# Kernel tuning notes

Measured on AMD Instinct MI355X. Metric: run time of the kernel, lower is better.

Reference implementation:

```python
import jax, jax.numpy as jnp
import numpy as np

BETA = 0.25  # commitment cost
EPS = 1e-10


def _vq_layer(xf, cb):
    # xf: [M, D] flattened features, cb: [K, D] codebook
    K = cb.shape[0]
    M = xf.shape[0]
    d = (jnp.sum(xf * xf, axis=-1, keepdims=True)
         - 2.0 * (xf @ cb.T)
         + jnp.sum(cb * cb, axis=-1))
    idx = jnp.argmin(d, axis=-1)          # [M]
    q = cb[idx]                           # [M, D]
    # commitment + codebook loss (VQ-VAE)
    commit = jnp.mean((jax.lax.stop_gradient(q) - xf) ** 2)
    cbloss = jnp.mean((q - jax.lax.stop_gradient(xf)) ** 2)
    loss = cbloss + BETA * commit
    # straight-through estimator
    q_st = xf + jax.lax.stop_gradient(q - xf)
    # codebook usage perplexity
    counts = jnp.zeros((K,), dtype=xf.dtype).at[idx].add(1.0)
    p = counts / M
    perplexity = jnp.exp(-jnp.sum(p * jnp.log(p + EPS)))
    return q_st, idx, loss, perplexity


def setup_inputs() -> dict:
    key = jax.random.key(0)
    k1, k2 = jax.random.split(key)
    B, N, D, H, W, K = 32, 4, 128, 32, 32, 1024
    x = jax.random.normal(k1, (B, N * D, H, W), dtype=jnp.float32)
    codebooks = jax.random.normal(k2, (N, K, D), dtype=jnp.float32)
    return {"x": x, "codebooks": codebooks}


def reference(x, codebooks):
    B, C, H, W = x.shape
    N, K, D = codebooks.shape
    assert C == N * D
    M = B * H * W
    # [B, N*D, H, W] -> [N, M, D]
    xs = x.reshape(B, N, D, H, W).transpose(1, 0, 3, 4, 2).reshape(N, M, D)
    q, idx, loss, perp = jax.vmap(_vq_layer)(xs, codebooks)
    # quantized_cat: [N, M, D] -> [B, N*D, H, W]  (cat along channel dim)
    quantized_cat = (q.reshape(N, B, H, W, D)
                      .transpose(1, 0, 4, 2, 3)
                      .reshape(B, N * D, H, W))
    # indices_cat: [N, M] -> [B, N, H, W]
    indices_cat = idx.reshape(N, B, H, W).transpose(1, 0, 2, 3)
    return quantized_cat, indices_cat, loss, perp
```

## Files before the change

kernel.cpp:

```cpp
#include <hip/hip_runtime.h>

#define B_ 32
#define N_ 4
#define D_ 128
#define M_ 32768
#define K_ 1024

#define IDX_OFF 16777216
#define LOSS_OFF 16908288
#define PERP_OFF 16908292

#define WS_LOSS 0
#define WS_CNT 1024
#define WS_ENORM 8192
#define WS_BPACK_F 16384
#define BPACK_LAYER_US 262144
#define WS_IDX 540672

#define SBIAS 384.0f
#define MARGIN 0.012f

typedef __bf16 bf16x8 __attribute__((ext_vector_type(8)));
typedef float f32x4 __attribute__((ext_vector_type(4)));

union FragU {
  bf16x8 v;
  ushort u16[8];
  uint4 q;
};

__device__ __forceinline__ ushort bf16_hi_rne(float f, float* hif) {
  uint u = __float_as_uint(f);
  uint r = (u + 0x7fffu + ((u >> 16) & 1u)) >> 16;
  *hif = __uint_as_float(r << 16);
  return (ushort)r;
}
__device__ __forceinline__ ushort bf16_rne(float f) {
  uint u = __float_as_uint(f);
  return (ushort)((u + 0x7fffu + ((u >> 16) & 1u)) >> 16);
}

__device__ __forceinline__ void gload_lds16(const void* g, void* l) {
  __builtin_amdgcn_global_load_lds(
      (const __attribute__((address_space(1))) unsigned int*)g,
      (__attribute__((address_space(3))) unsigned int*)l, 16, 0, 0);
}

__global__ __launch_bounds__(256) void vq_pack(const float* __restrict__ cb,
                                               float* __restrict__ ws) {
  __shared__ ushort Hs[16 * 132];
  __shared__ ushort Ls[16 * 132];
  __shared__ float Ps[256];
  int blk = blockIdx.x, tid = threadIdx.x;
  if (blk < 256) {
    int n = blk >> 6, tile = blk & 63;
    int c = tid >> 4, f = tid & 15;
    const float* src = cb + ((size_t)(n * K_ + tile * 16 + c)) * D_ + f * 8;
    float4 v0 = *(const float4*)src;
    float4 v1 = *(const float4*)(src + 4);
    float v[8] = {v0.x, v0.y, v0.z, v0.w, v1.x, v1.y, v1.z, v1.w};
    float ss = 0.f;
#pragma unroll
    for (int j = 0; j < 8; ++j) {
      float hif;
      Hs[c * 132 + f * 8 + j] = bf16_hi_rne(v[j], &hif);
      Ls[c * 132 + f * 8 + j] = bf16_rne(v[j] - hif);
      ss = fmaf(v[j], v[j], ss);
    }
    Ps[c * 16 + f] = ss;
    __syncthreads();
    if (tid < 16) {
      float s = 0.f;
#pragma unroll
      for (int j = 0; j < 16; ++j) s += Ps[tid * 16 + j];
      ws[WS_ENORM + n * K_ + tile * 16 + tid] = SBIAS - 0.5f * s;
    }
    int s = tid >> 6, lane = tid & 63;
    int code = lane & 15, dstart = s * 32 + ((lane >> 4) << 3);
    FragU fh, fl;
#pragma unroll
    for (int j = 0; j < 8; ++j) {
      fh.u16[j] = Hs[code * 132 + dstart + j];
      fl.u16[j] = Ls[code * 132 + dstart + j];
    }
    ushort* dst = (ushort*)(ws + WS_BPACK_F) + (size_t)n * BPACK_LAYER_US +
                  ((size_t)(tile * 4 + s) * 2) * 512 + lane * 8;
    *(uint4*)dst = fh.q;
    *(uint4*)(dst + 512) = fl.q;
  } else {
#pragma unroll
    for (int i = 0; i < 20; ++i) ws[i * 256 + tid] = 0.f;
  }
}

__global__ __launch_bounds__(256, 4) void vq_score(const float* __restrict__ x,
                                                   const float* __restrict__ cb,
                                                   float* __restrict__ ws,
                                                   float* __restrict__ out) {
  __shared__ alignas(16) ushort Bsm[18432];
  const int tid = threadIdx.x;
  const int bid = blockIdx.x;
  const int n = bid >> 8;
  const int mblk = bid & 255;
  const int b = mblk >> 3;
  const int hw0 = (mblk & 7) << 7;

  const int lane = tid & 63, w = tid >> 6;
  const int quad = lane >> 4, l15 = lane & 15;

  const float* xbase = x + (size_t)((b * 4 + n) * 128) * 1024 + hw0;
  const float* cbn = cb + (size_t)n * K_ * D_;
  const float* enB = ws + WS_ENORM + n * K_;
  const uint4* gsrc = (const uint4*)((ushort*)(ws + WS_BPACK_F) + (size_t)n * BPACK_LAYER_US);
  uint4* Bsm4 = (uint4*)Bsm;

  char* ext = (char*)Bsm + 32768;
  int* sIdx = (int*)ext;
  float* dist = (float*)(ext + 512);
  int* list = (int*)(ext + 1024);
  int* lcnt = (int*)(ext + 1536);
  double* xrowd = (double*)(ext + 1544);
  double* rd = (double*)(ext + 2568);
  int* rk = (int*)(ext + 2600);

  if (tid == 0) *lcnt = 0;

  bf16x8 ahi[2][4], alo[2][4];
#pragma unroll
  for (int set = 0; set < 2; ++set) {
    const int hwl = w * 32 + set * 16 + l15;
    float xs = 0.f;
#pragma unroll
    for (int s = 0; s < 4; ++s) {
      const int dbase = s * 32 + quad * 8;
      FragU fh, fl;
#pragma unroll
      for (int j = 0; j < 8; ++j) {
        float v = xbase[(size_t)(dbase + j) * 1024 + hwl];
        xs = fmaf(v, v, xs);
        float hif;
        fh.u16[j] = bf16_hi_rne(v, &hif);
        fl.u16[j] = bf16_rne(v - hif);
      }
      ahi[set][s] = fh.v;
      alo[set][s] = fl.v;
    }
    xs += __shfl_xor(xs, 16, 64);
    xs += __shfl_xor(xs, 32, 64);
    if (lane < 16) dist[w * 32 + set * 16 + l15] = xs;
  }

  uint best[8], best2[8], keyp[8];
#pragma unroll
  for (int i = 0; i < 8; ++i) { best[i] = 0u; best2[i] = 0u; keyp[i] = 0u; }

#pragma unroll
  for (int i = 0; i < 4; ++i)
    gload_lds16(gsrc + i * 256 + w * 64 + lane, Bsm4 + i * 256 + w * 64);

#pragma unroll 1
  for (int c = 0; c < 32; ++c) {
    __syncthreads();
    if (c < 31) {
      const uint4* src = gsrc + (c + 1) * 1024;
      uint4* dst = Bsm4 + ((c + 1) & 1) * 1024;
#pragma unroll
      for (int i = 0; i < 4; ++i)
        gload_lds16(src + i * 256 + w * 64 + lane, dst + i * 256 + w * 64);
    }
    const ushort* Bcur = Bsm + (c & 1) * 8192;
#pragma unroll
    for (int tin = 0; tin < 2; ++tin) {
      const int t = c * 2 + tin;
      const uint tinv = (uint)(63 - t);
      float en = enB[t * 16 + l15];
      bf16x8 bh[4], bl[4];
#pragma unroll
      for (int s = 0; s < 4; ++s) {
        const ushort* p = Bcur + ((tin * 4 + s) * 2) * 512 + lane * 8;
        bh[s] = ((const FragU*)p)->v;
        bl[s] = ((const FragU*)(p + 512))->v;
      }
      f32x4 acc[2];
#pragma unroll
      for (int set = 0; set < 2; ++set) acc[set] = (f32x4){0.f, 0.f, 0.f, 0.f};
#pragma unroll
      for (int s = 0; s < 4; ++s) {
#pragma unroll
        for (int set = 0; set < 2; ++set)
          acc[set] = __builtin_amdgcn_mfma_f32_16x16x32_bf16(ahi[set][s], bh[s], acc[set], 0, 0, 0);
#pragma unroll
        for (int set = 0; set < 2; ++set)
          acc[set] = __builtin_amdgcn_mfma_f32_16x16x32_bf16(ahi[set][s], bl[s], acc[set], 0, 0, 0);
#pragma unroll
        for (int set = 0; set < 2; ++set)
          acc[set] = __builtin_amdgcn_mfma_f32_16x16x32_bf16(alo[set][s], bh[s], acc[set], 0, 0, 0);
      }
#pragma unroll
      for (int i = 0; i < 8; ++i) {
        uint k = keyp[i], ob = best[i];
        uint mn = k < ob ? k : ob;
        best[i] = k > ob ? k : ob;
        if (mn > best2[i]) best2[i] = mn;
      }
#pragma unroll
      for (int set = 0; set < 2; ++set) {
#pragma unroll
        for (int r = 0; r < 4; ++r) {
          float sb = acc[set][r] + en;
          keyp[set * 4 + r] = (__float_as_uint(sb) & 0xFFFFFFC0u) | tinv;
        }
      }
    }
  }
#pragma unroll
  for (int i = 0; i < 8; ++i) {
    uint k = keyp[i], ob = best[i];
    uint mn = k < ob ? k : ob;
    best[i] = k > ob ? k : ob;
    if (mn > best2[i]) best2[i] = mn;
  }
  __syncthreads();

  uint* sS = (uint*)Bsm;
  uint* sS2 = (uint*)((char*)Bsm + 8704);
#pragma unroll
  for (int set = 0; set < 2; ++set) {
#pragma unroll
    for (int r = 0; r < 4; ++r) {
      int m = w * 32 + set * 16 + quad * 4 + r;
      sS[m * 17 + l15] = best[set * 4 + r];
      sS2[m * 17 + l15] = best2[set * 4 + r];
    }
  }
  __syncthreads();

  if (tid < 128) {
    int m = tid;
    uint g1 = 0, g2 = 0;
    int gi = 0;
#pragma unroll 4
    for (int li = 0; li < 16; ++li) {
      uint key = sS[m * 17 + li];
      uint sb = key >> 6;
      int kk = (int)(63u - (key & 63u)) * 16 + li;
      if (sb > g1) { g2 = g1; g1 = sb; gi = kk; }
      else {
        if (sb == g1 && kk < gi) gi = kk;
        if (sb > g2) g2 = sb;
      }
      uint sb2 = sS2[m * 17 + li] >> 6;
      if (sb2 > g2) g2 = sb2;
    }
    sIdx[m] = gi;
    float s1f = __uint_as_float(g1 << 6);
    dist[m] = dist[m] - 2.0f * (s1f - SBIAS);
    float gap = s1f - __uint_as_float(g2 << 6);
    if (gap < MARGIN) {
      int pos = atomicAdd(lcnt, 1);
      list[pos] = m;
    }
  }
  __syncthreads();

  const int cnt = *lcnt;
  for (int i = 0; i < cnt; ++i) {
    const int m = list[i];
    if (tid < 128) xrowd[tid] = (double)xbase[(size_t)tid * 1024 + m];
    __syncthreads();
    double bd = 1e300;
    int bk = 0;
#pragma unroll 1
    for (int j = 0; j < 4; ++j) {
      const int k = tid * 4 + j;
      const float4* er = (const float4*)(cbn + (size_t)k * D_);
      double d = 0.0;
#pragma unroll 8
      for (int c4 = 0; c4 < 32; ++c4) {
        float4 e = er[c4];
        double d0 = xrowd[c4 * 4 + 0] - (double)e.x;
        double d1 = xrowd[c4 * 4 + 1] - (double)e.y;
        double d2 = xrowd[c4 * 4 + 2] - (double)e.z;
        double d3 = xrowd[c4 * 4 + 3] - (double)e.w;
        d = fma(d0, d0, d);
        d = fma(d1, d1, d);
        d = fma(d2, d2, d);
        d = fma(d3, d3, d);
      }
      if (d < bd) { bd = d; bk = k; }
    }
#pragma unroll
    for (int off = 32; off; off >>= 1) {
      double od = __shfl_down(bd, off, 64);
      int ok = __shfl_down(bk, off, 64);
      if (od < bd || (od == bd && ok < bk)) { bd = od; bk = ok; }
    }
    if (lane == 0) { rd[w] = bd; rk[w] = bk; }
    __syncthreads();
    if (tid == 0) {
      double gb = rd[0];
      int gk = rk[0];
      for (int t = 1; t < 4; ++t)
        if (rd[t] < gb || (rd[t] == gb && rk[t] < gk)) { gb = rd[t]; gk = rk[t]; }
      sIdx[m] = gk;
      dist[m] = (float)gb;
    }
    __syncthreads();
  }

  if (tid < 128) {
    int bi = sIdx[tid];
    int gpos = (b * 4 + n) * 1024 + hw0 + tid;
    out[IDX_OFF + gpos] = (float)bi;
    ((int*)(ws + WS_IDX))[gpos] = bi;
    atomicAdd(ws + WS_CNT + n * K_ + bi, 1.0f);
  }
  float lp = (tid < 128) ? dist[tid] : 0.f;
#pragma unroll
  for (int off = 32; off; off >>= 1) lp += __shfl_down(lp, off, 64);
  if (lane == 0 && w < 2) atomicAdd(ws + WS_LOSS + n, lp);
}

__global__ __launch_bounds__(256) void vq_write(const float* __restrict__ cb,
                                                const float* __restrict__ ws,
                                                float* __restrict__ out) {
  __shared__ float Qs[32 * 128];
  __shared__ int sIdx[128];
  const int tid = threadIdx.x;
  const int bid = blockIdx.x;
  const int n = bid >> 8;
  const int mblk = bid & 255;
  const int b = mblk >> 3;
  const int hw0 = (mblk & 7) << 7;
  const float* cbn = cb + (size_t)n * K_ * D_;
  const int* ig = (const int*)(ws + WS_IDX) + (b * 4 + n) * 1024 + hw0;
  if (tid < 128) sIdx[tid] = ig[tid];
  __syncthreads();
  float* out0 = out + (size_t)((b * 4 + n) * 128) * 1024 + hw0;
#pragma unroll 1
  for (int q = 0; q < 4; ++q) {
    const int m = tid & 127, part = tid >> 7;
    const float* src = cbn + (size_t)sIdx[m] * D_ + q * 32 + part * 16;
#pragma unroll
    for (int i = 0; i < 4; ++i) {
      float4 v = ((const float4*)src)[i];
      int dl = part * 16 + i * 4;
      Qs[(dl + 0) * 128 + m] = v.x;
      Qs[(dl + 1) * 128 + m] = v.y;
      Qs[(dl + 2) * 128 + m] = v.z;
      Qs[(dl + 3) * 128 + m] = v.w;
    }
    __syncthreads();
#pragma unroll
    for (int it = 0; it < 4; ++it) {
      int e = it * 256 + tid;
      int m4 = (e & 31) * 4;
      int dl = e >> 5;
      float4 v = *(float4*)(Qs + dl * 128 + m4);
      *(float4*)(out0 + (size_t)(q * 32 + dl) * 1024 + m4) = v;
    }
    __syncthreads();
  }
}

__global__ void vq_finalize(const float* __restrict__ ws, float* __restrict__ out) {
  int n = blockIdx.x;
  int t = threadIdx.x;
  const float* counts = ws + WS_CNT + n * K_;
  float s = 0.f;
  for (int k = t; k < K_; k += 256) {
    float p = counts[k] * (1.0f / 32768.0f);
    s += p * logf(p + 1e-10f);
  }
  __shared__ float red[4];
#pragma unroll
  for (int off = 32; off; off >>= 1) s += __shfl_down(s, off, 64);
  if ((t & 63) == 0) red[t >> 6] = s;
  __syncthreads();
  if (t == 0) {
    s = red[0] + red[1] + red[2] + red[3];
    out[PERP_OFF + n] = expf(-s);
    out[LOSS_OFF + n] = 1.25f * ws[WS_LOSS + n] / 4194304.0f;
  }
}

extern "C" void kernel_launch(void* const* d_in, const int* in_sizes, int n_in,
                              void* d_out, int out_size, void* d_ws, size_t ws_size,
                              hipStream_t stream) {
  const float* x = (const float*)d_in[0];
  const float* cb = (const float*)d_in[1];
  float* out = (float*)d_out;
  float* ws = (float*)d_ws;
  vq_pack<<<257, 256, 0, stream>>>(cb, ws);
  vq_score<<<1024, 256, 0, stream>>>(x, cb, ws, out);
  vq_write<<<1024, 256, 0, stream>>>(cb, ws, out);
  vq_finalize<<<4, 256, 0, stream>>>(ws, out);
}
```

Measured before the change: 296.9 us.

## Fuse scoring and quantized write into one kernel with 256-row blocks

```diff
diff --git a/kernel.cpp b/kernel.cpp
--- a/kernel.cpp
+++ b/kernel.cpp
@@ -15,7 +15,6 @@
 #define WS_ENORM 8192
 #define WS_BPACK_F 16384
 #define BPACK_LAYER_US 262144
-#define WS_IDX 540672
 
 #define SBIAS 384.0f
 #define MARGIN 0.012f
@@ -93,17 +92,17 @@
   }
 }
 
-__global__ __launch_bounds__(256, 4) void vq_score(const float* __restrict__ x,
-                                                   const float* __restrict__ cb,
-                                                   float* __restrict__ ws,
-                                                   float* __restrict__ out) {
-  __shared__ alignas(16) ushort Bsm[18432];
+__global__ __launch_bounds__(512, 4) void vq_main(const float* __restrict__ x,
+                                                  const float* __restrict__ cb,
+                                                  float* __restrict__ ws,
+                                                  float* __restrict__ out) {
+  __shared__ alignas(16) char Lds[37120];
   const int tid = threadIdx.x;
   const int bid = blockIdx.x;
-  const int n = bid >> 8;
-  const int mblk = bid & 255;
-  const int b = mblk >> 3;
-  const int hw0 = (mblk & 7) << 7;
+  const int n = bid >> 7;
+  const int mblk = bid & 127;
+  const int b = mblk >> 2;
+  const int hw0 = (mblk & 3) << 8;
 
   const int lane = tid & 63, w = tid >> 6;
   const int quad = lane >> 4, l15 = lane & 15;
@@ -112,16 +111,18 @@
   const float* cbn = cb + (size_t)n * K_ * D_;
   const float* enB = ws + WS_ENORM + n * K_;
   const uint4* gsrc = (const uint4*)((ushort*)(ws + WS_BPACK_F) + (size_t)n * BPACK_LAYER_US);
-  uint4* Bsm4 = (uint4*)Bsm;
-
-  char* ext = (char*)Bsm + 32768;
+
+  ushort* Bsm = (ushort*)Lds;
+  uint4* Bsm4 = (uint4*)Lds;
+  char* ext = Lds + 32896;
   int* sIdx = (int*)ext;
-  float* dist = (float*)(ext + 512);
-  int* list = (int*)(ext + 1024);
-  int* lcnt = (int*)(ext + 1536);
-  double* xrowd = (double*)(ext + 1544);
-  double* rd = (double*)(ext + 2568);
-  int* rk = (int*)(ext + 2600);
+  float* dist = (float*)(ext + 1024);
+  int* list = (int*)(ext + 2048);
+  int* lcnt = (int*)(ext + 3072);
+  double* xrowd = (double*)(ext + 3080);
+  double* rd = (double*)(ext + 4104);
+  int* rk = (int*)(ext + 4168);
+  float* Qs = (float*)Lds;
 
   if (tid == 0) *lcnt = 0;
 
@@ -155,8 +156,8 @@
   for (int i = 0; i < 8; ++i) { best[i] = 0u; best2[i] = 0u; keyp[i] = 0u; }
 
 #pragma unroll
-  for (int i = 0; i < 4; ++i)
-    gload_lds16(gsrc + i * 256 + w * 64 + lane, Bsm4 + i * 256 + w * 64);
+  for (int i = 0; i < 2; ++i)
+    gload_lds16(gsrc + w * 128 + i * 64 + lane, Bsm4 + w * 128 + i * 64);
 
 #pragma unroll 1
   for (int c = 0; c < 32; ++c) {
@@ -165,8 +166,8 @@
       const uint4* src = gsrc + (c + 1) * 1024;
       uint4* dst = Bsm4 + ((c + 1) & 1) * 1024;
 #pragma unroll
-      for (int i = 0; i < 4; ++i)
-        gload_lds16(src + i * 256 + w * 64 + lane, dst + i * 256 + w * 64);
+      for (int i = 0; i < 2; ++i)
+        gload_lds16(src + w * 128 + i * 64 + lane, dst + w * 128 + i * 64);
     }
     const ushort* Bcur = Bsm + (c & 1) * 8192;
 #pragma unroll
@@ -220,45 +221,39 @@
     best[i] = k > ob ? k : ob;
     if (mn > best2[i]) best2[i] = mn;
   }
-  __syncthreads();
-
-  uint* sS = (uint*)Bsm;
-  uint* sS2 = (uint*)((char*)Bsm + 8704);
-#pragma unroll
-  for (int set = 0; set < 2; ++set) {
-#pragma unroll
-    for (int r = 0; r < 4; ++r) {
-      int m = w * 32 + set * 16 + quad * 4 + r;
-      sS[m * 17 + l15] = best[set * 4 + r];
-      sS2[m * 17 + l15] = best2[set * 4 + r];
-    }
-  }
-  __syncthreads();
-
-  if (tid < 128) {
-    int m = tid;
-    uint g1 = 0, g2 = 0;
-    int gi = 0;
-#pragma unroll 4
-    for (int li = 0; li < 16; ++li) {
-      uint key = sS[m * 17 + li];
-      uint sb = key >> 6;
-      int kk = (int)(63u - (key & 63u)) * 16 + li;
-      if (sb > g1) { g2 = g1; g1 = sb; gi = kk; }
-      else {
-        if (sb == g1 && kk < gi) gi = kk;
-        if (sb > g2) g2 = sb;
-      }
-      uint sb2 = sS2[m * 17 + li] >> 6;
-      if (sb2 > g2) g2 = sb2;
-    }
-    sIdx[m] = gi;
-    float s1f = __uint_as_float(g1 << 6);
-    dist[m] = dist[m] - 2.0f * (s1f - SBIAS);
-    float gap = s1f - __uint_as_float(g2 << 6);
-    if (gap < MARGIN) {
-      int pos = atomicAdd(lcnt, 1);
-      list[pos] = m;
+
+  uint pre[8];
+#pragma unroll
+  for (int i = 0; i < 8; ++i) pre[i] = best[i];
+#pragma unroll
+  for (int off = 1; off < 16; off <<= 1) {
+#pragma unroll
+    for (int i = 0; i < 8; ++i) {
+      uint o1 = __shfl_xor(best[i], off, 16);
+      uint o2 = __shfl_xor(best2[i], off, 16);
+      uint mn = best[i] < o1 ? best[i] : o1;
+      best[i] = best[i] > o1 ? best[i] : o1;
+      uint mx2 = best2[i] > o2 ? best2[i] : o2;
+      best2[i] = mn > mx2 ? mn : mx2;
+    }
+  }
+#pragma unroll
+  for (int i = 0; i < 8; ++i) {
+    bool hit = (pre[i] == best[i]);
+    unsigned long long bal = __ballot(hit);
+    if (l15 == 0) {
+      uint grp = (uint)(bal >> (quad * 16)) & 0xFFFFu;
+      int wl = __builtin_ctz(grp);
+      int t = 63 - (int)(best[i] & 63u);
+      int m = w * 32 + (i >> 2) * 16 + quad * 4 + (i & 3);
+      sIdx[m] = t * 16 + wl;
+      float s1f = __uint_as_float(best[i] & 0xFFFFFFC0u);
+      float s2f = __uint_as_float(best2[i] & 0xFFFFFFC0u);
+      dist[m] = dist[m] - 2.0f * (s1f - SBIAS);
+      if (s1f - s2f < MARGIN) {
+        int pos = atomicAdd(lcnt, 1);
+        list[pos] = m;
+      }
     }
   }
   __syncthreads();
@@ -271,8 +266,8 @@
     double bd = 1e300;
     int bk = 0;
 #pragma unroll 1
-    for (int j = 0; j < 4; ++j) {
-      const int k = tid * 4 + j;
+    for (int j = 0; j < 2; ++j) {
+      const int k = tid * 2 + j;
       const float4* er = (const float4*)(cbn + (size_t)k * D_);
       double d = 0.0;
 #pragma unroll 8
@@ -300,7 +295,7 @@
     if (tid == 0) {
       double gb = rd[0];
       int gk = rk[0];
-      for (int t = 1; t < 4; ++t)
+      for (int t = 1; t < 8; ++t)
         if (rd[t] < gb || (rd[t] == gb && rk[t] < gk)) { gb = rd[t]; gk = rk[t]; }
       sIdx[m] = gk;
       dist[m] = (float)gb;
@@ -308,55 +303,38 @@
     __syncthreads();
   }
 
-  if (tid < 128) {
+  if (tid < 256) {
     int bi = sIdx[tid];
-    int gpos = (b * 4 + n) * 1024 + hw0 + tid;
-    out[IDX_OFF + gpos] = (float)bi;
-    ((int*)(ws + WS_IDX))[gpos] = bi;
+    out[IDX_OFF + (b * 4 + n) * 1024 + hw0 + tid] = (float)bi;
     atomicAdd(ws + WS_CNT + n * K_ + bi, 1.0f);
   }
-  float lp = (tid < 128) ? dist[tid] : 0.f;
+  float lp = (tid < 256) ? dist[tid] : 0.f;
 #pragma unroll
   for (int off = 32; off; off >>= 1) lp += __shfl_down(lp, off, 64);
-  if (lane == 0 && w < 2) atomicAdd(ws + WS_LOSS + n, lp);
-}
-
-__global__ __launch_bounds__(256) void vq_write(const float* __restrict__ cb,
-                                                const float* __restrict__ ws,
-                                                float* __restrict__ out) {
-  __shared__ float Qs[32 * 128];
-  __shared__ int sIdx[128];
-  const int tid = threadIdx.x;
-  const int bid = blockIdx.x;
-  const int n = bid >> 8;
-  const int mblk = bid & 255;
-  const int b = mblk >> 3;
-  const int hw0 = (mblk & 7) << 7;
-  const float* cbn = cb + (size_t)n * K_ * D_;
-  const int* ig = (const int*)(ws + WS_IDX) + (b * 4 + n) * 1024 + hw0;
-  if (tid < 128) sIdx[tid] = ig[tid];
+  if (lane == 0 && w < 4) atomicAdd(ws + WS_LOSS + n, lp);
   __syncthreads();
+
   float* out0 = out + (size_t)((b * 4 + n) * 128) * 1024 + hw0;
 #pragma unroll 1
   for (int q = 0; q < 4; ++q) {
-    const int m = tid & 127, part = tid >> 7;
+    const int m = tid & 255, part = tid >> 8;
     const float* src = cbn + (size_t)sIdx[m] * D_ + q * 32 + part * 16;
 #pragma unroll
     for (int i = 0; i < 4; ++i) {
       float4 v = ((const float4*)src)[i];
       int dl = part * 16 + i * 4;
-      Qs[(dl + 0) * 128 + m] = v.x;
-      Qs[(dl + 1) * 128 + m] = v.y;
-      Qs[(dl + 2) * 128 + m] = v.z;
-      Qs[(dl + 3) * 128 + m] = v.w;
+      Qs[(dl + 0) * 257 + m] = v.x;
+      Qs[(dl + 1) * 257 + m] = v.y;
+      Qs[(dl + 2) * 257 + m] = v.z;
+      Qs[(dl + 3) * 257 + m] = v.w;
     }
     __syncthreads();
 #pragma unroll
     for (int it = 0; it < 4; ++it) {
-      int e = it * 256 + tid;
-      int m4 = (e & 31) * 4;
-      int dl = e >> 5;
-      float4 v = *(float4*)(Qs + dl * 128 + m4);
+      int e = it * 512 + tid;
+      int m4 = (e & 63) * 4;
+      int dl = e >> 6;
+      float4 v = *(float4*)(Qs + dl * 257 + m4);
       *(float4*)(out0 + (size_t)(q * 32 + dl) * 1024 + m4) = v;
     }
     __syncthreads();
@@ -392,7 +370,6 @@
   float* out = (float*)d_out;
   float* ws = (float*)d_ws;
   vq_pack<<<257, 256, 0, stream>>>(cb, ws);
-  vq_score<<<1024, 256, 0, stream>>>(x, cb, ws, out);
-  vq_write<<<1024, 256, 0, stream>>>(cb, ws, out);
+  vq_main<<<512, 512, 0, stream>>>(x, cb, ws, out);
   vq_finalize<<<4, 256, 0, stream>>>(ws, out);
 }
```

After: 296.5 us. Within noise of the previous version (-0.1%).
